# Optimization experiments

Hardware: AMD Instinct MI355X
Metric: run time of the kernel (lower is better)

Reference implementation:

```python
import jax, jax.numpy as jnp
import numpy as np

EMBED_DIM = 1024
NUM_HEADS = 16
HEAD_DIM = EMBED_DIM // NUM_HEADS
SCALE = HEAD_DIM ** -0.5


def setup_inputs() -> dict:
    key = jax.random.key(0)
    ks = jax.random.split(key, 13)
    B, Q, K, E = 2, 1024, 2048, EMBED_DIM
    bound = 1.0 / np.sqrt(E)
    def lin(k1, k2):
        W = jax.random.uniform(k1, (E, E), jnp.float32, -bound, bound)
        b = jax.random.uniform(k2, (E,), jnp.float32, -bound, bound)
        return W, b
    Wq, bq = lin(ks[0], ks[1])
    Wk, bk = lin(ks[2], ks[3])
    Wv, bv = lin(ks[4], ks[5])
    Wo, bo = lin(ks[6], ks[7])
    return {
        "query": jax.random.normal(ks[8], (B, Q, E), jnp.float32),
        "key": jax.random.normal(ks[9], (B, K, E), jnp.float32),
        "value": jax.random.normal(ks[10], (B, K, E), jnp.float32),
        "key_padding_mask": jax.random.randint(ks[11], (B, K), 0, 2).astype(bool),
        "Wq": Wq, "bq": bq, "Wk": Wk, "bk": bk,
        "Wv": Wv, "bv": bv, "Wo": Wo, "bo": bo,
    }


def reference(query, key, value, key_padding_mask, Wq, bq, Wk, bk, Wv, bv, Wo, bo):
    B, Q, E = query.shape
    K = key.shape[1]
    H, D = NUM_HEADS, HEAD_DIM
    # projections (torch Linear: x @ W.T + b)
    q = (query @ Wq.T + bq).reshape(B, Q, H, D).transpose(0, 2, 1, 3)  # [B,H,Q,D]
    k = (key @ Wk.T + bk).reshape(B, K, H, D).transpose(0, 2, 1, 3)    # [B,H,K,D]
    v = (value @ Wv.T + bv).reshape(B, K, H, D).transpose(0, 2, 1, 3)  # [B,H,K,D]
    logits = jnp.einsum('bhqd,bhkd->bhqk', q, k) * SCALE               # [B,H,Q,K]
    logits = jnp.where(key_padding_mask[:, None, None, :], -jnp.inf, logits)
    attn = jax.nn.softmax(logits, axis=-1)
    out = jnp.einsum('bhqk,bhkd->bhqd', attn, v)                        # [B,H,Q,D]
    out = out.transpose(0, 2, 1, 3).reshape(B, Q, E)
    out = out @ Wo.T + bo
    return out
```

## Files before the change

### kernel.cpp

```cpp
#include <hip/hip_runtime.h>

typedef __bf16 bf16_t;
typedef __bf16 bf16x4 __attribute__((ext_vector_type(4)));
typedef __bf16 bf16x8 __attribute__((ext_vector_type(8)));
typedef float f32x4 __attribute__((ext_vector_type(4)));

#define B_ 2
#define H_ 16
#define D_ 64
#define E_ 1024
#define QL 1024
#define KL 2048
#define SCALE_L2E 0.1803368801111204f
#define NEG_BIG -1e30f

__device__ __forceinline__ void gload_lds16(const void* g, void* lds) {
  auto* gp = reinterpret_cast<const __attribute__((address_space(1))) uint32_t*>(
      reinterpret_cast<uintptr_t>(g));
  auto* lp = reinterpret_cast<__attribute__((address_space(3))) uint32_t*>(
      reinterpret_cast<uintptr_t>(lds));
  __builtin_amdgcn_global_load_lds(gp, lp, 16, 0, 0);
}

__global__ __launch_bounds__(256) void cast_bf16_k(const float* __restrict__ in,
                                                   bf16_t* __restrict__ out) {
  size_t i = (size_t)blockIdx.x * 256 + threadIdx.x;
  float4 a = ((const float4*)in)[2 * i];
  float4 b = ((const float4*)in)[2 * i + 1];
  bf16x8 o;
  o[0] = (bf16_t)a.x; o[1] = (bf16_t)a.y; o[2] = (bf16_t)a.z; o[3] = (bf16_t)a.w;
  o[4] = (bf16_t)b.x; o[5] = (bf16_t)b.y; o[6] = (bf16_t)b.z; o[7] = (bf16_t)b.w;
  ((bf16x8*)out)[i] = o;
}

__global__ __launch_bounds__(256) void cast4_k(const float* __restrict__ w0, const float* __restrict__ w1,
                                               const float* __restrict__ w2, const float* __restrict__ w3,
                                               bf16_t* __restrict__ o0, bf16_t* __restrict__ o1,
                                               bf16_t* __restrict__ o2, bf16_t* __restrict__ o3) {
  int seg = blockIdx.y;
  const float* in = (seg == 0) ? w0 : (seg == 1) ? w1 : (seg == 2) ? w2 : w3;
  bf16_t* out = (seg == 0) ? o0 : (seg == 1) ? o1 : (seg == 2) ? o2 : o3;
  size_t i = (size_t)blockIdx.x * 256 + threadIdx.x;
  float4 a = ((const float4*)in)[2 * i];
  float4 b = ((const float4*)in)[2 * i + 1];
  bf16x8 o;
  o[0] = (bf16_t)a.x; o[1] = (bf16_t)a.y; o[2] = (bf16_t)a.z; o[3] = (bf16_t)a.w;
  o[4] = (bf16_t)b.x; o[5] = (bf16_t)b.y; o[6] = (bf16_t)b.z; o[7] = (bf16_t)b.w;
  ((bf16x8*)out)[i] = o;
}

__global__ void prep_mask(const unsigned char* __restrict__ mraw, float* __restrict__ bias) {
  __shared__ int flagMis, flagB0;
  int t = threadIdx.x;
  if (t == 0) { flagMis = 0; flagB0 = 0; }
  __syncthreads();
  int a = 0, c = 0;
  for (int i = t; i < B_ * KL; i += 256) {
    if (i & 3) a |= mraw[i]; else c |= mraw[i];
  }
  if (a) atomicOr(&flagMis, 1);
  if (c) atomicOr(&flagB0, 1);
  __syncthreads();
  int mode = (flagMis == 0) ? 0 : (flagB0 ? 1 : 2);
  for (int i = t; i < B_ * KL; i += 256) {
    int mv;
    if (mode == 0)      mv = ((const int*)mraw)[i];
    else if (mode == 1) mv = mraw[i];
    else                mv = (((const float*)mraw)[i] != 0.0f);
    bias[i] = mv ? NEG_BIG : 0.0f;
  }
}

template <int MODE>
__global__ __launch_bounds__(256, 2)
void gemm_nt(const bf16_t* __restrict__ A, const bf16_t* __restrict__ W,
             const float* __restrict__ bias, void* __restrict__ Cout,
             int M, int N, int K, int Lshift) {
  __shared__ alignas(16) bf16_t As[2][128 * 64];
  __shared__ alignas(16) bf16_t Bs[2][128 * 64];
  const int tid = threadIdx.x;
  const int lane = tid & 63;
  const int w = tid >> 6;
  const int l15 = lane & 15, l4 = lane >> 4;
  const int wr = w >> 1, wc = w & 1;
  const int row0 = blockIdx.x * 128, col0 = blockIdx.y * 128;

  f32x4 acc[4][4] = {};

  auto stage = [&](int buf, int kt) {
    const int k0 = kt * 64;
#pragma unroll
    for (int i = 0; i < 4; ++i) {
      int idx = (w * 4 + i) * 64 + lane;
      int r = idx >> 3, c = idx & 7;
      int cs = ((c ^ (r & 7)) * 8);
      gload_lds16(A + (size_t)(row0 + r) * K + k0 + cs, &As[buf][(w * 4 + i) * 512]);
      gload_lds16(W + (size_t)(col0 + r) * K + k0 + cs, &Bs[buf][(w * 4 + i) * 512]);
    }
  };

  auto compute = [&](int buf) {
#pragma unroll
    for (int t = 0; t < 2; ++t) {
      bf16x8 af[4], bfv[4];
#pragma unroll
      for (int i = 0; i < 4; ++i) {
        int r = wr * 64 + i * 16 + l15;
        af[i] = *(const bf16x8*)&As[buf][r * 64 + (((t * 4 + l4) ^ (r & 7)) * 8)];
      }
#pragma unroll
      for (int j = 0; j < 4; ++j) {
        int r = wc * 64 + j * 16 + l15;
        bfv[j] = *(const bf16x8*)&Bs[buf][r * 64 + (((t * 4 + l4) ^ (r & 7)) * 8)];
      }
#pragma unroll
      for (int i = 0; i < 4; ++i)
#pragma unroll
        for (int j = 0; j < 4; ++j)
          acc[i][j] = __builtin_amdgcn_mfma_f32_16x16x32_bf16(af[i], bfv[j], acc[i][j], 0, 0, 0);
    }
  };

  stage(0, 0);
  const int nk = K >> 6;
  for (int kt = 0; kt < nk; ++kt) {
    __syncthreads();
    if (kt + 1 < nk) stage((kt + 1) & 1, kt + 1);
    compute(kt & 1);
  }

#pragma unroll
  for (int i = 0; i < 4; ++i) {
    int mbase = row0 + wr * 64 + i * 16 + l4 * 4;
    f32x4 bvm = {};
    if (MODE == 2) bvm = *(const f32x4*)&bias[mbase];
#pragma unroll
    for (int j = 0; j < 4; ++j) {
      int n = col0 + wc * 64 + j * 16 + l15;
      float bv = (MODE == 2) ? 0.f : bias[n];
#pragma unroll
      for (int r = 0; r < 4; ++r) {
        float v = acc[i][j][r] + ((MODE == 2) ? bvm[r] : bv);
        int m = mbase + r;
        if (MODE == 0) {
          int bi = m >> Lshift;
          int ml = m & ((1 << Lshift) - 1);
          size_t dst = ((((size_t)bi * H_ + (n >> 6)) << Lshift) + ml) * D_ + (n & 63);
          ((bf16_t*)Cout)[dst] = (bf16_t)v;
        } else if (MODE == 1) {
          ((float*)Cout)[(size_t)m * N + n] = v;
        } else {
          int hh = m >> 6, d = m & 63;
          int bi = n >> 11, k = n & (KL - 1);
          ((bf16_t*)Cout)[((((size_t)bi * H_ + hh) << 6) + d) * KL + k] = (bf16_t)v;
        }
      }
    }
  }
}

__global__ __launch_bounds__(128, 2)
void attn_fused(const bf16_t* __restrict__ qh, const bf16_t* __restrict__ kh,
                const bf16_t* __restrict__ vhT, const float* __restrict__ mbias,
                bf16_t* __restrict__ outx) {
  __shared__ alignas(16) bf16_t Ksm[2][64 * 64];
  __shared__ alignas(16) bf16_t Vt[2][64 * 64];
  __shared__ alignas(16) bf16_t Ps[2][16 * 64];

  const int qt = blockIdx.x, h = blockIdx.y, b = blockIdx.z;
  const int tid = threadIdx.x, lane = tid & 63, w = tid >> 6;
  const int l15 = lane & 15, l4 = lane >> 4;
  const size_t bh = (size_t)b * H_ + h;

  const bf16_t* qbase = qh + (bh * QL + qt * 32 + w * 16) * D_;
  bf16x8 qf[2];
#pragma unroll
  for (int t = 0; t < 2; ++t)
    qf[t] = *(const bf16x8*)(qbase + l15 * D_ + t * 32 + l4 * 8);

  float m_run = NEG_BIG, l_run = 0.f;
  f32x4 o_acc[4] = {};

  const bf16_t* kbase = kh + bh * KL * D_;
  const bf16_t* vtb = vhT + bh * (size_t)D_ * KL;
  const float* mrow = mbias + (size_t)b * KL;

  auto stage = [&](int bufsel, int kt) {
#pragma unroll
    for (int i = 0; i < 4; ++i) {
      int idx = (w * 4 + i) * 64 + lane;
      int r = idx >> 3, c = idx & 7;
      int cs = (c ^ (r & 7)) * 8;
      gload_lds16(kbase + (size_t)(kt * 64 + r) * D_ + cs, &Ksm[bufsel][idx * 8]);
      gload_lds16(vtb + (size_t)r * KL + kt * 64 + cs, &Vt[bufsel][idx * 8]);
    }
  };

  stage(0, 0);
  __syncthreads();

  for (int kt = 0; kt < KL / 64; ++kt) {
    const int buf = kt & 1;
    if (kt + 1 < KL / 64) stage(buf ^ 1, kt + 1);

    f32x4 mv[4];
#pragma unroll
    for (int ct = 0; ct < 4; ++ct)
      mv[ct] = *(const f32x4*)&mrow[kt * 64 + ct * 16 + l4 * 4];

    f32x4 s[4] = {};
#pragma unroll
    for (int ct = 0; ct < 4; ++ct) {
      int krow = ct * 16 + l15;
#pragma unroll
      for (int t = 0; t < 2; ++t) {
        bf16x8 kf = *(const bf16x8*)&Ksm[buf][krow * 64 + (((t * 4 + l4) ^ (krow & 7)) * 8)];
        s[ct] = __builtin_amdgcn_mfma_f32_16x16x32_bf16(kf, qf[t], s[ct], 0, 0, 0);
      }
    }

    float sv[4][4];
    float mt = NEG_BIG;
#pragma unroll
    for (int ct = 0; ct < 4; ++ct)
#pragma unroll
      for (int r = 0; r < 4; ++r) {
        float x = s[ct][r] * SCALE_L2E + mv[ct][r];
        sv[ct][r] = x;
        mt = fmaxf(mt, x);
      }
    mt = fmaxf(mt, __shfl_xor(mt, 16, 64));
    mt = fmaxf(mt, __shfl_xor(mt, 32, 64));
    float mnew = fmaxf(m_run, mt);
    float alpha = exp2f(m_run - mnew);
    m_run = mnew;
    float rsum = 0.f;
#pragma unroll
    for (int ct = 0; ct < 4; ++ct)
#pragma unroll
      for (int r = 0; r < 4; ++r) {
        float p = exp2f(sv[ct][r] - mnew);
        sv[ct][r] = p;
        rsum += p;
      }
    rsum += __shfl_xor(rsum, 16, 64);
    rsum += __shfl_xor(rsum, 32, 64);
    l_run = l_run * alpha + rsum;

    char* psrow = (char*)&Ps[w][0] + l15 * 128;
#pragma unroll
    for (int ct = 0; ct < 4; ++ct) {
      bf16x4 pk;
#pragma unroll
      for (int r = 0; r < 4; ++r) pk[r] = (bf16_t)sv[ct][r];
      *(bf16x4*)(psrow + (((ct * 4 + l4) ^ l15) * 8)) = pk;
    }

    float arow[4];
#pragma unroll
    for (int r = 0; r < 4; ++r) arow[r] = __shfl(alpha, l4 * 4 + r, 64);
#pragma unroll
    for (int dt = 0; dt < 4; ++dt)
#pragma unroll
      for (int r = 0; r < 4; ++r) o_acc[dt][r] *= arow[r];

#pragma unroll
    for (int t = 0; t < 2; ++t) {
      int c0 = t * 8 + l4 * 2;
      bf16x4 plo = *(const bf16x4*)(psrow + ((c0 ^ l15) * 8));
      bf16x4 phi = *(const bf16x4*)(psrow + (((c0 + 1) ^ l15) * 8));
      bf16x8 pa;
#pragma unroll
      for (int j = 0; j < 4; ++j) { pa[j] = plo[j]; pa[j + 4] = phi[j]; }
#pragma unroll
      for (int dt = 0; dt < 4; ++dt) {
        int d = dt * 16 + l15;
        bf16x8 vf = *(const bf16x8*)&Vt[buf][d * 64 + (((t * 4 + l4) ^ (d & 7)) * 8)];
        o_acc[dt] = __builtin_amdgcn_mfma_f32_16x16x32_bf16(pa, vf, o_acc[dt], 0, 0, 0);
      }
    }
    __syncthreads();
  }

  float inv = 1.0f / l_run;
  float irow[4];
#pragma unroll
  for (int r = 0; r < 4; ++r) irow[r] = __shfl(inv, l4 * 4 + r, 64);
#pragma unroll
  for (int r = 0; r < 4; ++r) {
    int qrow = qt * 32 + w * 16 + l4 * 4 + r;
#pragma unroll
    for (int dt = 0; dt < 4; ++dt) {
      int d = dt * 16 + l15;
      outx[((size_t)b * QL + qrow) * E_ + h * D_ + d] = (bf16_t)(o_acc[dt][r] * irow[r]);
    }
  }
}

extern "C" void kernel_launch(void* const* d_in, const int* in_sizes, int n_in,
                              void* d_out, int out_size, void* d_ws, size_t ws_size,
                              hipStream_t stream) {
  const float* query = (const float*)d_in[0];
  const float* key   = (const float*)d_in[1];
  const float* value = (const float*)d_in[2];
  const void*  mask  = d_in[3];
  const float* Wq = (const float*)d_in[4];
  const float* bq = (const float*)d_in[5];
  const float* Wk = (const float*)d_in[6];
  const float* bk = (const float*)d_in[7];
  const float* Wv = (const float*)d_in[8];
  const float* bv = (const float*)d_in[9];
  const float* Wo = (const float*)d_in[10];
  const float* bo = (const float*)d_in[11];

  char* ws = (char*)d_ws;
  bf16_t* Xq  = (bf16_t*)(ws + (0ull  << 20));
  bf16_t* Xk  = (bf16_t*)(ws + (4ull  << 20));
  bf16_t* Xv  = (bf16_t*)(ws + (12ull << 20));
  bf16_t* Wqb = (bf16_t*)(ws + (20ull << 20));
  bf16_t* Wkb = (bf16_t*)(ws + (22ull << 20));
  bf16_t* Wvb = (bf16_t*)(ws + (24ull << 20));
  bf16_t* Wob = (bf16_t*)(ws + (26ull << 20));
  bf16_t* qhd = (bf16_t*)(ws + (28ull << 20));
  bf16_t* khd = (bf16_t*)(ws + (32ull << 20));
  bf16_t* vht = (bf16_t*)(ws + (40ull << 20));
  bf16_t* axo = (bf16_t*)(ws + (48ull << 20));
  float*  mbias = (float*)(ws + (52ull << 20));

  dim3 blk(256);
  prep_mask<<<1, blk, 0, stream>>>((const unsigned char*)mask, mbias);
  cast_bf16_k<<<(2 * QL * E_) / 2048, blk, 0, stream>>>(query, Xq);
  cast_bf16_k<<<(2 * KL * E_) / 2048, blk, 0, stream>>>(key, Xk);
  cast_bf16_k<<<(2 * KL * E_) / 2048, blk, 0, stream>>>(value, Xv);
  cast4_k<<<dim3((E_ * E_) / 2048, 4), blk, 0, stream>>>(Wq, Wk, Wv, Wo, Wqb, Wkb, Wvb, Wob);

  gemm_nt<0><<<dim3(16, 8), blk, 0, stream>>>(Xq, Wqb, bq, qhd, 2048, 1024, 1024, 10);
  gemm_nt<0><<<dim3(32, 8), blk, 0, stream>>>(Xk, Wkb, bk, khd, 4096, 1024, 1024, 11);
  gemm_nt<2><<<dim3(8, 32), blk, 0, stream>>>(Wvb, Xv, bv, vht, 1024, 4096, 1024, 0);

  attn_fused<<<dim3(QL / 32, H_, B_), dim3(128), 0, stream>>>(qhd, khd, vht, mbias, axo);

  gemm_nt<1><<<dim3(16, 8), blk, 0, stream>>>(axo, Wob, bo, (float*)d_out, 2048, 1024, 1024, 0);
}
```

Baseline: 232.6 us.

## Merge cast and QKV GEMM launches, defer softmax rescale, add XCD-aware block remap

Folds the four cast kernels into one launch and the three projection GEMMs into a single 640-block launch. In both the QKV GEMM and attention, block indices are remapped so neighbouring work lands on the same XCD. In the attention loop, the running-max update and output rescale now run only when some lane's tile max exceeds the running max by more than a threshold. Row-sum shuffles are moved out of the loop to a single reduction at the end, and s_setprio is raised around the MFMA sections. The aim is less launch overhead, better cache locality, and fewer exp/shuffle/rescale operations per tile. The cost is more branching and reliance on the threshold staying within fp32/bf16 range.

```diff
diff --git a/kernel.cpp b/kernel.cpp
--- a/kernel.cpp
+++ b/kernel.cpp
@@ -13,6 +13,7 @@
 #define KL 2048
 #define SCALE_L2E 0.1803368801111204f
 #define NEG_BIG -1e30f
+#define DEFER_THR 8.0f
 
 __device__ __forceinline__ void gload_lds16(const void* g, void* lds) {
   auto* gp = reinterpret_cast<const __attribute__((address_space(1))) uint32_t*>(
@@ -22,25 +23,23 @@
   __builtin_amdgcn_global_load_lds(gp, lp, 16, 0, 0);
 }
 
-__global__ __launch_bounds__(256) void cast_bf16_k(const float* __restrict__ in,
-                                                   bf16_t* __restrict__ out) {
-  size_t i = (size_t)blockIdx.x * 256 + threadIdx.x;
-  float4 a = ((const float4*)in)[2 * i];
-  float4 b = ((const float4*)in)[2 * i + 1];
-  bf16x8 o;
-  o[0] = (bf16_t)a.x; o[1] = (bf16_t)a.y; o[2] = (bf16_t)a.z; o[3] = (bf16_t)a.w;
-  o[4] = (bf16_t)b.x; o[5] = (bf16_t)b.y; o[6] = (bf16_t)b.z; o[7] = (bf16_t)b.w;
-  ((bf16x8*)out)[i] = o;
-}
-
-__global__ __launch_bounds__(256) void cast4_k(const float* __restrict__ w0, const float* __restrict__ w1,
-                                               const float* __restrict__ w2, const float* __restrict__ w3,
-                                               bf16_t* __restrict__ o0, bf16_t* __restrict__ o1,
-                                               bf16_t* __restrict__ o2, bf16_t* __restrict__ o3) {
-  int seg = blockIdx.y;
-  const float* in = (seg == 0) ? w0 : (seg == 1) ? w1 : (seg == 2) ? w2 : w3;
-  bf16_t* out = (seg == 0) ? o0 : (seg == 1) ? o1 : (seg == 2) ? o2 : o3;
-  size_t i = (size_t)blockIdx.x * 256 + threadIdx.x;
+__global__ __launch_bounds__(256) void cast_all(
+    const float* __restrict__ q, const float* __restrict__ k, const float* __restrict__ v,
+    const float* __restrict__ wq, const float* __restrict__ wk,
+    const float* __restrict__ wv, const float* __restrict__ wo,
+    bf16_t* __restrict__ oq, bf16_t* __restrict__ ok, bf16_t* __restrict__ ov,
+    bf16_t* __restrict__ owq, bf16_t* __restrict__ owk,
+    bf16_t* __restrict__ owv, bf16_t* __restrict__ owo) {
+  int blk = blockIdx.x;
+  const float* in; bf16_t* out; int base;
+  if (blk < 1024)      { in = q;  out = oq;  base = blk; }
+  else if (blk < 3072) { in = k;  out = ok;  base = blk - 1024; }
+  else if (blk < 5120) { in = v;  out = ov;  base = blk - 3072; }
+  else if (blk < 5632) { in = wq; out = owq; base = blk - 5120; }
+  else if (blk < 6144) { in = wk; out = owk; base = blk - 5632; }
+  else if (blk < 6656) { in = wv; out = owv; base = blk - 6144; }
+  else                 { in = wo; out = owo; base = blk - 6656; }
+  size_t i = (size_t)base * 256 + threadIdx.x;
   float4 a = ((const float4*)in)[2 * i];
   float4 b = ((const float4*)in)[2 * i + 1];
   bf16x8 o;
@@ -68,6 +67,114 @@
     else if (mode == 1) mv = mraw[i];
     else                mv = (((const float*)mraw)[i] != 0.0f);
     bias[i] = mv ? NEG_BIG : 0.0f;
+  }
+}
+
+__global__ __launch_bounds__(256, 2)
+void qkv_gemm(const bf16_t* __restrict__ Xq, const bf16_t* __restrict__ Xk,
+              const bf16_t* __restrict__ Xv, const bf16_t* __restrict__ Wqb,
+              const bf16_t* __restrict__ Wkb, const bf16_t* __restrict__ Wvb,
+              const float* __restrict__ bq, const float* __restrict__ bk,
+              const float* __restrict__ bv,
+              bf16_t* __restrict__ qhd, bf16_t* __restrict__ khd, bf16_t* __restrict__ vht) {
+  __shared__ alignas(16) bf16_t As[2][128 * 64];
+  __shared__ alignas(16) bf16_t Bs[2][128 * 64];
+  const int wid = blockIdx.x;
+  const int work = (wid & 7) * 80 + (wid >> 3);
+
+  const bf16_t *A, *W;
+  const float* bias;
+  bf16_t* out;
+  int mode, Lshift, row0, col0;
+  if (work < 128) {
+    A = Xq; W = Wqb; bias = bq; out = qhd; mode = 0; Lshift = 10;
+    row0 = (work >> 3) * 128; col0 = (work & 7) * 128;
+  } else if (work < 384) {
+    int t = work - 128;
+    A = Xk; W = Wkb; bias = bk; out = khd; mode = 0; Lshift = 11;
+    row0 = (t >> 3) * 128; col0 = (t & 7) * 128;
+  } else {
+    int t = work - 384;
+    A = Wvb; W = Xv; bias = bv; out = vht; mode = 2; Lshift = 0;
+    row0 = (t & 7) * 128; col0 = (t >> 3) * 128;
+  }
+
+  const int K = 1024;
+  const int tid = threadIdx.x;
+  const int lane = tid & 63;
+  const int w = tid >> 6;
+  const int l15 = lane & 15, l4 = lane >> 4;
+  const int wr = w >> 1, wc = w & 1;
+
+  f32x4 acc[4][4] = {};
+
+  auto stage = [&](int buf, int kt) {
+    const int k0 = kt * 64;
+#pragma unroll
+    for (int i = 0; i < 4; ++i) {
+      int idx = (w * 4 + i) * 64 + lane;
+      int r = idx >> 3, c = idx & 7;
+      int cs = ((c ^ (r & 7)) * 8);
+      gload_lds16(A + (size_t)(row0 + r) * K + k0 + cs, &As[buf][(w * 4 + i) * 512]);
+      gload_lds16(W + (size_t)(col0 + r) * K + k0 + cs, &Bs[buf][(w * 4 + i) * 512]);
+    }
+  };
+
+  auto compute = [&](int buf) {
+#pragma unroll
+    for (int t = 0; t < 2; ++t) {
+      bf16x8 af[4], bfv[4];
+#pragma unroll
+      for (int i = 0; i < 4; ++i) {
+        int r = wr * 64 + i * 16 + l15;
+        af[i] = *(const bf16x8*)&As[buf][r * 64 + (((t * 4 + l4) ^ (r & 7)) * 8)];
+      }
+#pragma unroll
+      for (int j = 0; j < 4; ++j) {
+        int r = wc * 64 + j * 16 + l15;
+        bfv[j] = *(const bf16x8*)&Bs[buf][r * 64 + (((t * 4 + l4) ^ (r & 7)) * 8)];
+      }
+#pragma unroll
+      for (int i = 0; i < 4; ++i)
+#pragma unroll
+        for (int j = 0; j < 4; ++j)
+          acc[i][j] = __builtin_amdgcn_mfma_f32_16x16x32_bf16(af[i], bfv[j], acc[i][j], 0, 0, 0);
+    }
+  };
+
+  stage(0, 0);
+  const int nk = K >> 6;
+  for (int kt = 0; kt < nk; ++kt) {
+    __syncthreads();
+    if (kt + 1 < nk) stage((kt + 1) & 1, kt + 1);
+    compute(kt & 1);
+  }
+
+#pragma unroll
+  for (int i = 0; i < 4; ++i) {
+    int mbase = row0 + wr * 64 + i * 16 + l4 * 4;
+    f32x4 bvm = {};
+    if (mode == 2) bvm = *(const f32x4*)&bias[mbase];
+#pragma unroll
+    for (int j = 0; j < 4; ++j) {
+      int n = col0 + wc * 64 + j * 16 + l15;
+      float bv = (mode == 2) ? 0.f : bias[n];
+#pragma unroll
+      for (int r = 0; r < 4; ++r) {
+        float v = acc[i][j][r] + ((mode == 2) ? bvm[r] : bv);
+        int m = mbase + r;
+        if (mode == 0) {
+          int bi = m >> Lshift;
+          int ml = m & ((1 << Lshift) - 1);
+          size_t dst = ((((size_t)bi * H_ + (n >> 6)) << Lshift) + ml) * D_ + (n & 63);
+          out[dst] = (bf16_t)v;
+        } else {
+          int hh = m >> 6, d = m & 63;
+          int bi = n >> 11, kk = n & (KL - 1);
+          out[((((size_t)bi * H_ + hh) << 6) + d) * KL + kk] = (bf16_t)v;
+        }
+      }
+    }
   }
 }
 
@@ -132,28 +239,15 @@
 #pragma unroll
   for (int i = 0; i < 4; ++i) {
     int mbase = row0 + wr * 64 + i * 16 + l4 * 4;
-    f32x4 bvm = {};
-    if (MODE == 2) bvm = *(const f32x4*)&bias[mbase];
 #pragma unroll
     for (int j = 0; j < 4; ++j) {
       int n = col0 + wc * 64 + j * 16 + l15;
-      float bv = (MODE == 2) ? 0.f : bias[n];
+      float bv = bias[n];
 #pragma unroll
       for (int r = 0; r < 4; ++r) {
-        float v = acc[i][j][r] + ((MODE == 2) ? bvm[r] : bv);
+        float v = acc[i][j][r] + bv;
         int m = mbase + r;
-        if (MODE == 0) {
-          int bi = m >> Lshift;
-          int ml = m & ((1 << Lshift) - 1);
-          size_t dst = ((((size_t)bi * H_ + (n >> 6)) << Lshift) + ml) * D_ + (n & 63);
-          ((bf16_t*)Cout)[dst] = (bf16_t)v;
-        } else if (MODE == 1) {
-          ((float*)Cout)[(size_t)m * N + n] = v;
-        } else {
-          int hh = m >> 6, d = m & 63;
-          int bi = n >> 11, k = n & (KL - 1);
-          ((bf16_t*)Cout)[((((size_t)bi * H_ + hh) << 6) + d) * KL + k] = (bf16_t)v;
-        }
+        ((float*)Cout)[(size_t)m * N + n] = v;
       }
     }
   }
@@ -167,12 +261,17 @@
   __shared__ alignas(16) bf16_t Vt[2][64 * 64];
   __shared__ alignas(16) bf16_t Ps[2][16 * 64];
 
-  const int qt = blockIdx.x, h = blockIdx.y, b = blockIdx.z;
+  const int wid = blockIdx.x;
+  const int work = (wid & 7) * 128 + (wid >> 3);
+  const int qt = work & 31;
+  const int bh = work >> 5;
+  const int h = bh & 15, b = bh >> 4;
+
   const int tid = threadIdx.x, lane = tid & 63, w = tid >> 6;
   const int l15 = lane & 15, l4 = lane >> 4;
-  const size_t bh = (size_t)b * H_ + h;
-
-  const bf16_t* qbase = qh + (bh * QL + qt * 32 + w * 16) * D_;
+  const size_t bhs = (size_t)b * H_ + h;
+
+  const bf16_t* qbase = qh + (bhs * QL + qt * 32 + w * 16) * D_;
   bf16x8 qf[2];
 #pragma unroll
   for (int t = 0; t < 2; ++t)
@@ -181,8 +280,8 @@
   float m_run = NEG_BIG, l_run = 0.f;
   f32x4 o_acc[4] = {};
 
-  const bf16_t* kbase = kh + bh * KL * D_;
-  const bf16_t* vtb = vhT + bh * (size_t)D_ * KL;
+  const bf16_t* kbase = kh + bhs * KL * D_;
+  const bf16_t* vtb = vhT + bhs * (size_t)D_ * KL;
   const float* mrow = mbias + (size_t)b * KL;
 
   auto stage = [&](int bufsel, int kt) {
@@ -209,6 +308,7 @@
       mv[ct] = *(const f32x4*)&mrow[kt * 64 + ct * 16 + l4 * 4];
 
     f32x4 s[4] = {};
+    __builtin_amdgcn_s_setprio(1);
 #pragma unroll
     for (int ct = 0; ct < 4; ++ct) {
       int krow = ct * 16 + l15;
@@ -218,6 +318,7 @@
         s[ct] = __builtin_amdgcn_mfma_f32_16x16x32_bf16(kf, qf[t], s[ct], 0, 0, 0);
       }
     }
+    __builtin_amdgcn_s_setprio(0);
 
     float sv[4][4];
     float mt = NEG_BIG;
@@ -229,23 +330,33 @@
         sv[ct][r] = x;
         mt = fmaxf(mt, x);
       }
-    mt = fmaxf(mt, __shfl_xor(mt, 16, 64));
-    mt = fmaxf(mt, __shfl_xor(mt, 32, 64));
-    float mnew = fmaxf(m_run, mt);
-    float alpha = exp2f(m_run - mnew);
-    m_run = mnew;
+
+    if (!__all(mt <= m_run + DEFER_THR)) {
+      mt = fmaxf(mt, __shfl_xor(mt, 16, 64));
+      mt = fmaxf(mt, __shfl_xor(mt, 32, 64));
+      float mnew = fmaxf(m_run, mt);
+      float alpha = exp2f(m_run - mnew);
+      m_run = mnew;
+      l_run *= alpha;
+      float arow[4];
+#pragma unroll
+      for (int r = 0; r < 4; ++r) arow[r] = __shfl(alpha, l4 * 4 + r, 64);
+#pragma unroll
+      for (int dt = 0; dt < 4; ++dt)
+#pragma unroll
+        for (int r = 0; r < 4; ++r) o_acc[dt][r] *= arow[r];
+    }
+
     float rsum = 0.f;
 #pragma unroll
     for (int ct = 0; ct < 4; ++ct)
 #pragma unroll
       for (int r = 0; r < 4; ++r) {
-        float p = exp2f(sv[ct][r] - mnew);
+        float p = exp2f(sv[ct][r] - m_run);
         sv[ct][r] = p;
         rsum += p;
       }
-    rsum += __shfl_xor(rsum, 16, 64);
-    rsum += __shfl_xor(rsum, 32, 64);
-    l_run = l_run * alpha + rsum;
+    l_run += rsum;
 
     char* psrow = (char*)&Ps[w][0] + l15 * 128;
 #pragma unroll
@@ -256,14 +367,7 @@
       *(bf16x4*)(psrow + (((ct * 4 + l4) ^ l15) * 8)) = pk;
     }
 
-    float arow[4];
-#pragma unroll
-    for (int r = 0; r < 4; ++r) arow[r] = __shfl(alpha, l4 * 4 + r, 64);
-#pragma unroll
-    for (int dt = 0; dt < 4; ++dt)
-#pragma unroll
-      for (int r = 0; r < 4; ++r) o_acc[dt][r] *= arow[r];
-
+    __builtin_amdgcn_s_setprio(1);
 #pragma unroll
     for (int t = 0; t < 2; ++t) {
       int c0 = t * 8 + l4 * 2;
@@ -279,10 +383,13 @@
         o_acc[dt] = __builtin_amdgcn_mfma_f32_16x16x32_bf16(pa, vf, o_acc[dt], 0, 0, 0);
       }
     }
+    __builtin_amdgcn_s_setprio(0);
     __syncthreads();
   }
 
-  float inv = 1.0f / l_run;
+  float l_tot = l_run + __shfl_xor(l_run, 16, 64);
+  l_tot += __shfl_xor(l_tot, 32, 64);
+  float inv = 1.0f / l_tot;
   float irow[4];
 #pragma unroll
   for (int r = 0; r < 4; ++r) irow[r] = __shfl(inv, l4 * 4 + r, 64);
@@ -327,18 +434,12 @@
   bf16_t* axo = (bf16_t*)(ws + (48ull << 20));
   float*  mbias = (float*)(ws + (52ull << 20));
 
-  dim3 blk(256);
-  prep_mask<<<1, blk, 0, stream>>>((const unsigned char*)mask, mbias);
-  cast_bf16_k<<<(2 * QL * E_) / 2048, blk, 0, stream>>>(query, Xq);
-  cast_bf16_k<<<(2 * KL * E_) / 2048, blk, 0, stream>>>(key, Xk);
-  cast_bf16_k<<<(2 * KL * E_) / 2048, blk, 0, stream>>>(value, Xv);
-  cast4_k<<<dim3((E_ * E_) / 2048, 4), blk, 0, stream>>>(Wq, Wk, Wv, Wo, Wqb, Wkb, Wvb, Wob);
-
-  gemm_nt<0><<<dim3(16, 8), blk, 0, stream>>>(Xq, Wqb, bq, qhd, 2048, 1024, 1024, 10);
-  gemm_nt<0><<<dim3(32, 8), blk, 0, stream>>>(Xk, Wkb, bk, khd, 4096, 1024, 1024, 11);
-  gemm_nt<2><<<dim3(8, 32), blk, 0, stream>>>(Wvb, Xv, bv, vht, 1024, 4096, 1024, 0);
-
-  attn_fused<<<dim3(QL / 32, H_, B_), dim3(128), 0, stream>>>(qhd, khd, vht, mbias, axo);
-
-  gemm_nt<1><<<dim3(16, 8), blk, 0, stream>>>(axo, Wob, bo, (float*)d_out, 2048, 1024, 1024, 0);
-}
+  prep_mask<<<1, 256, 0, stream>>>((const unsigned char*)mask, mbias);
+  cast_all<<<7168, 256, 0, stream>>>(query, key, value, Wq, Wk, Wv, Wo,
+                                     Xq, Xk, Xv, Wqb, Wkb, Wvb, Wob);
+  qkv_gemm<<<640, 256, 0, stream>>>(Xq, Xk, Xv, Wqb, Wkb, Wvb, bq, bk, bv,
+                                    qhd, khd, vht);
+  attn_fused<<<1024, 128, 0, stream>>>(qhd, khd, vht, mbias, axo);
+  gemm_nt<1><<<dim3(16, 8), 256, 0, stream>>>(axo, Wob, bo, (float*)d_out,
+                                              2048, 1024, 1024, 0);
+}
```

Result: faster. 211.3 us (-9.2%).
